# Optimization experiments

Measured on AMD Instinct MI355X. Metric: run time of the kernel, lower is better.

Reference implementation:

```python
import jax, jax.numpy as jnp
import numpy as np
from jax import lax

B, N, C_IN, C_OUT = 8, 8192, 64, 128
NUM_SAMPLES, K = 2048, 32
EPS = 1e-5


def _bn(x, g, b, m, v):
    # inference-mode BatchNorm1d over channel axis 1; x: [G, C, L]
    scale = g / jnp.sqrt(v + EPS)
    return (x - m[None, :, None]) * scale[None, :, None] + b[None, :, None]


def _conv1x1(x, w):
    # kernel_size=1 Conv1d (no bias); x: [G, Cin, L], w: [Cout, Cin]
    return jnp.einsum('gck,oc->gok', x, w)


def _res_block(x, w1, g1, b1, m1, v1, w2, g2, b2, m2, v2):
    # conv-bn-relu -> conv-bn, residual add, relu (residual_factor=1.0)
    y = jax.nn.relu(_bn(_conv1x1(x, w1), g1, b1, m1, v1))
    y = _bn(_conv1x1(y, w2), g2, b2, m2, v2)
    return jax.nn.relu(y + x)


def _fps(xyz, num_samples):
    # farthest point sampling; xyz: [B,N,3] -> indices [B,S]
    b, n, _ = xyz.shape

    def step(carry, _):
        dists, last_idx = carry
        last_pt = jnp.take_along_axis(xyz, last_idx[:, None, None], axis=1)  # [B,1,3]
        d = jnp.sum((xyz - last_pt) ** 2, axis=-1)  # [B,N]
        dists = jnp.minimum(dists, d)
        nxt = jnp.argmax(dists, axis=-1).astype(jnp.int32)
        return (dists, nxt), last_idx

    init = (jnp.full((b, n), 1e10, xyz.dtype), jnp.zeros((b,), jnp.int32))
    _, idxs = lax.scan(step, init, None, length=num_samples)
    return jnp.transpose(idxs)  # [B,S]


def setup_inputs():
    key = jax.random.key(0)
    ks = jax.random.split(key, 40)
    xyz = jax.random.uniform(ks[0], (B, N, 3), jnp.float32)
    feat = jax.random.normal(ks[1], (B, N, C_IN), jnp.float32)

    def conv_w(k, o, c):
        return jax.random.normal(k, (o, c), jnp.float32) * (1.0 / np.sqrt(c).astype(np.float32))

    def bn_params(k, c):
        k1, k2, k3, k4 = jax.random.split(k, 4)
        return (1.0 + 0.1 * jax.random.normal(k1, (c,), jnp.float32),
                0.1 * jax.random.normal(k2, (c,), jnp.float32),
                0.1 * jax.random.normal(k3, (c,), jnp.float32),
                jax.random.uniform(k4, (c,), jnp.float32, 0.5, 1.5))

    inp = {'xyz': xyz, 'feat': feat}
    inp['te_w'] = conv_w(ks[2], C_OUT, 2 * C_IN)
    inp['te_g'], inp['te_b'], inp['te_m'], inp['te_v'] = bn_params(ks[3], C_OUT)
    for name, base in (('pre', 4), ('pos', 14)):
        inp[name + '_w1'] = jnp.stack([conv_w(ks[base + i], C_OUT, C_OUT) for i in range(2)])
        inp[name + '_w2'] = jnp.stack([conv_w(ks[base + 2 + i], C_OUT, C_OUT) for i in range(2)])
        bn1 = [bn_params(ks[base + 4 + i], C_OUT) for i in range(2)]
        bn2 = [bn_params(ks[base + 6 + i], C_OUT) for i in range(2)]
        for j, s in enumerate(('g', 'b', 'm', 'v')):
            inp[f'{name}_{s}1'] = jnp.stack([bn1[i][j] for i in range(2)])
            inp[f'{name}_{s}2'] = jnp.stack([bn2[i][j] for i in range(2)])
    return inp


def reference(xyz, feat, te_w, te_g, te_b, te_m, te_v,
              pre_w1, pre_w2, pre_g1, pre_b1, pre_m1, pre_v1, pre_g2, pre_b2, pre_m2, pre_v2,
              pos_w1, pos_w2, pos_g1, pos_b1, pos_m1, pos_v1, pos_g2, pos_b2, pos_m2, pos_v2):
    bsz = xyz.shape[0]
    # --- LocalGrouper: FPS centers + kNN grouping + concat center feat ---
    fps_idx = _fps(xyz, NUM_SAMPLES)                                    # [B,S]
    new_xyz = jnp.take_along_axis(xyz, fps_idx[..., None], axis=1)      # [B,S,3]
    ctr_feat = jnp.take_along_axis(feat, fps_idx[..., None], axis=1)    # [B,S,C]
    d2 = jnp.sum((new_xyz[:, :, None, :] - xyz[:, None, :, :]) ** 2, axis=-1)  # [B,S,N]
    _, knn_idx = lax.top_k(-d2, K)                                      # [B,S,K]
    grouped = feat[jnp.arange(bsz)[:, None, None], knn_idx]             # [B,S,K,C]
    ctr = jnp.broadcast_to(ctr_feat[:, :, None, :], grouped.shape)
    nf = jnp.concatenate([grouped, ctr], axis=-1)                       # [B,S,K,2C]
    # --- permute/view -> [B*S, 2C, K] ---
    x = nf.transpose(0, 1, 3, 2).reshape(bsz * NUM_SAMPLES, 2 * C_IN, K)
    x = jax.nn.relu(_bn(_conv1x1(x, te_w), te_g, te_b, te_m, te_v))     # [G,OUT,K]
    for i in range(2):
        x = _res_block(x, pre_w1[i], pre_g1[i], pre_b1[i], pre_m1[i], pre_v1[i],
                       pre_w2[i], pre_g2[i], pre_b2[i], pre_m2[i], pre_v2[i])
    x = jnp.max(x, axis=-1)                                             # adaptive_max_pool1d(.,1)
    x = x.reshape(bsz, NUM_SAMPLES, C_OUT).transpose(0, 2, 1)           # [B,OUT,S]
    for i in range(2):
        x = _res_block(x, pos_w1[i], pos_g1[i], pos_b1[i], pos_m1[i], pos_v1[i],
                       pos_w2[i], pos_g2[i], pos_b2[i], pos_m2[i], pos_v2[i])
    return new_xyz, x
```

## Files before the change

kernel.cpp:

```cpp
#include <hip/hip_runtime.h>

typedef unsigned short u16;
typedef unsigned int   u32;
typedef unsigned long long u64;

#define B_    8
#define N_    8192
#define CIN   64
#define COUT  128
#define NS    2048
#define K_    32
#define LDSPAD 136

typedef __attribute__((ext_vector_type(8))) short short8;
typedef __attribute__((ext_vector_type(4))) float f32x4;
typedef __attribute__((ext_vector_type(2))) float f32x2;

#define MFMA16(a,b,c) __builtin_amdgcn_mfma_f32_16x16x32_bf16(a,b,c,0,0,0)

__device__ __forceinline__ u16 f2bf(float f){
  u32 u = __float_as_uint(f);
  return (u16)((u + 0x7FFFu + ((u >> 16) & 1u)) >> 16);
}
__device__ __forceinline__ float bf2f(u16 h){ u32 u = ((u32)h) << 16; return __uint_as_float(u); }
__device__ __forceinline__ u32 pack2bf(float lo, float hi){ return (u32)f2bf(lo) | ((u32)f2bf(hi) << 16); }

__global__ void clear_kernel(int* __restrict__ fps_idx, u32* __restrict__ done,
                             u32* __restrict__ wready){
  int i = blockIdx.x * 256 + threadIdx.x;
  if (i < B_*NS){ fps_idx[i] = -1; done[i] = 0u; }
  if (i == 0) wready[0] = 0u;
}

struct BnPtrs { const float* g[9]; const float* b[9]; const float* m[9]; const float* v[9]; };

struct ShFps {
  u64 key3[3];
  __align__(16) f32x4 cA[2][8];
};
struct ShMid {
  __align__(16) u16 X[8][32*LDSPAD];
  __align__(16) float scr[8][128];
};
struct ShPos {
  __align__(16) u16 X[8][32*LDSPAD];
};
union ShAll { ShFps f; ShMid m; ShPos p; char pad[83968]; };

__device__ __forceinline__ void lds_barrier(){
  __builtin_amdgcn_sched_barrier(0);
  asm volatile("s_waitcnt lgkmcnt(0)\n\ts_barrier" ::: "memory");
  __builtin_amdgcn_sched_barrier(0);
}

#define DPP_UMAX(x, ctrl) { \
  u32 o = (u32)__builtin_amdgcn_update_dpp((int)(x), (int)(x), ctrl, 0xf, 0xf, false); \
  x = (o > x) ? o : x; }

__device__ __forceinline__ u32 wave_umax63(u32 x){
  DPP_UMAX(x, 0x111)
  DPP_UMAX(x, 0x112)
  DPP_UMAX(x, 0x114)
  DPP_UMAX(x, 0x118)
  DPP_UMAX(x, 0x142)
  DPP_UMAX(x, 0x143)
  return (u32)__builtin_amdgcn_readlane((int)x, 63);
}

#define FPS_PAIR(m) { \
  f32x2 dx = PXr##m - lx2; \
  f32x2 dy = PYr##m - ly2; \
  f32x2 dz = PZr##m - lz2; \
  f32x2 t0 = dx*dx; \
  f32x2 t1 = dy*dy; \
  f32x2 t2 = dz*dz; \
  f32x2 dd = (t0 + t1) + t2; \
  f32x2 nd; \
  nd.x = fminf(Dr##m.x, dd.x); \
  nd.y = fminf(Dr##m.y, dd.y); \
  Dr##m = nd; \
  fmA = fmaxf(fmA, nd.x); \
  fmB = fmaxf(fmB, nd.y); }

#define FPS_SELK(m) { \
  if (Dr##m.y == wmf){ kk = 2*m + 1; wx = PXr##m.y; wy = PYr##m.y; wz = PZr##m.y; } \
  if (Dr##m.x == wmf){ kk = 2*m;     wx = PXr##m.x; wy = PYr##m.x; wz = PZr##m.x; } }

__device__ void fps_path(const float* __restrict__ xyz, int* __restrict__ fps_idx,
                         ShFps& S, int b, int t){
  #pragma clang fp contract(off)
  const int lane = t & 63, wv = t >> 6;
  const float* xb = xyz + (size_t)b * N_ * 3;
  const int base = t * 16;
  f32x4 raw0, raw1, raw2, raw3, raw4, raw5, raw6, raw7, raw8, raw9, rawA, rawB;
  {
    const f32x4* xv = (const f32x4*)(xb + (size_t)base * 3);
    raw0 = xv[0]; raw1 = xv[1]; raw2 = xv[2];  raw3 = xv[3];
    raw4 = xv[4]; raw5 = xv[5]; raw6 = xv[6];  raw7 = xv[7];
    raw8 = xv[8]; raw9 = xv[9]; rawA = xv[10]; rawB = xv[11];
  }
  f32x2 PXr0,PXr1,PXr2,PXr3,PXr4,PXr5,PXr6,PXr7;
  f32x2 PYr0,PYr1,PYr2,PYr3,PYr4,PYr5,PYr6,PYr7;
  f32x2 PZr0,PZr1,PZr2,PZr3,PZr4,PZr5,PZr6,PZr7;
  #define GETF(k) (k<4?raw0[(k)&3]:k<8?raw1[(k)&3]:k<12?raw2[(k)&3]:k<16?raw3[(k)&3]: \
                   k<20?raw4[(k)&3]:k<24?raw5[(k)&3]:k<28?raw6[(k)&3]:k<32?raw7[(k)&3]: \
                   k<36?raw8[(k)&3]:k<40?raw9[(k)&3]:k<44?rawA[(k)&3]:rawB[(k)&3])
  #define SETP(m) { \
    PXr##m.x = GETF(6*m+0); PXr##m.y = GETF(6*m+3); \
    PYr##m.x = GETF(6*m+1); PYr##m.y = GETF(6*m+4); \
    PZr##m.x = GETF(6*m+2); PZr##m.y = GETF(6*m+5); }
  SETP(0) SETP(1) SETP(2) SETP(3) SETP(4) SETP(5) SETP(6) SETP(7)
  #undef SETP
  #undef GETF
  if (t == 0){
    S.key3[0] = 0; S.key3[1] = 0; S.key3[2] = 0;
    __hip_atomic_store(fps_idx + b*NS, 0, __ATOMIC_RELAXED, __HIP_MEMORY_SCOPE_AGENT);
  }
  f32x2 Dr0,Dr1,Dr2,Dr3,Dr4,Dr5,Dr6,Dr7;
  Dr0=Dr1=Dr2=Dr3=Dr4=Dr5=Dr6=Dr7=(f32x2){1e10f,1e10f};
  const float sx = xb[0], sy = xb[1], sz = xb[2];
  f32x2 lx2 = {sx,sx}, ly2 = {sy,sy}, lz2 = {sz,sz};
  __syncthreads();
  int my_pi = 0;
  int sl3 = 0, zsl = 1;
  for (int s = 0; s < NS - 1; ++s){
    float fmA = 0.f, fmB = 0.f;
    FPS_PAIR(0) FPS_PAIR(1) FPS_PAIR(2) FPS_PAIR(3)
    FPS_PAIR(4) FPS_PAIR(5) FPS_PAIR(6) FPS_PAIR(7)
    const float fm = fmaxf(fmA, fmB);
    const u32 tbm = __float_as_uint(fm);
    const u32 wmax = wave_umax63(tbm);
    const u64 mask = __ballot(tbm == wmax);
    const int fl = __ffsll((long long)mask) - 1;
    const int sl = s & 1;
    if (lane == fl){
      const float wmf = __uint_as_float(wmax);
      int kk = 0;
      float wx = PXr0.x, wy = PYr0.x, wz = PZr0.x;
      FPS_SELK(7) FPS_SELK(6) FPS_SELK(5) FPS_SELK(4)
      FPS_SELK(3) FPS_SELK(2) FPS_SELK(1) FPS_SELK(0)
      const int pi = base + kk;
      atomicMax((unsigned long long*)&S.key3[sl3],
                ((u64)wmax << 13) | (u64)(8191 - pi));
      f32x4 c; c[0] = wx; c[1] = wy; c[2] = wz; c[3] = 0.f;
      S.cA[sl][wv] = c;
    }
    if (t == 0) S.key3[zsl] = 0;
    lds_barrier();
    const u64 win = S.key3[sl3];
    const int pi_out = 8191 - (int)(win & 0x1FFFull);
    const f32x4 c0 = S.cA[sl][pi_out >> 10];
    lx2.x = c0[0]; lx2.y = c0[0];
    ly2.x = c0[1]; ly2.y = c0[1];
    lz2.x = c0[2]; lz2.y = c0[2];
    if (lane == (s & 15)) my_pi = pi_out;
    if ((s & 15) == 15 && t < 16)
      __hip_atomic_store(fps_idx + b*NS + s - 14 + t, my_pi,
                         __ATOMIC_RELAXED, __HIP_MEMORY_SCOPE_AGENT);
    sl3 = zsl; zsl = (zsl == 2) ? 0 : (zsl + 1);
  }
  if (t < 15)
    __hip_atomic_store(fps_idx + b*NS + (NS - 15) + t, my_pi,
                       __ATOMIC_RELAXED, __HIP_MEMORY_SCOPE_AGENT);
}

__device__ __forceinline__ void st_wt(u32* p, u32 v){
  __hip_atomic_store(p, v, __ATOMIC_RELAXED, __HIP_MEMORY_SCOPE_AGENT);
}

__device__ void prep_path(const float* s_te, const float* s_pre1, const float* s_pre2,
    const float* s_pos1, const float* s_pos2,
    u16* te_w, u16* pre_w1, u16* pre_w2, u16* pos_w1, u16* pos_w2,
    BnPtrs bp, float* bns, u32* wready, int t){
  #define CVT2(src, dst, n) \
    for (int i = t; i < (n)/2; i += 512) \
      st_wt((u32*)(dst) + i, pack2bf((src)[2*i], (src)[2*i+1]));
  CVT2(s_te,   te_w,   16384)
  CVT2(s_pre1, pre_w1, 32768)
  CVT2(s_pre2, pre_w2, 32768)
  CVT2(s_pos1, pos_w1, 32768)
  CVT2(s_pos2, pos_w2, 32768)
  #undef CVT2
  for (int i = t; i < 9*128; i += 512){
    int set = i >> 7, c = i & 127;
    float sc = bp.g[set][c] / sqrtf(bp.v[set][c] + 1e-5f);
    st_wt((u32*)(bns + set*256 + c),       __float_as_uint(sc));
    st_wt((u32*)(bns + set*256 + 128 + c), __float_as_uint(bp.b[set][c] - bp.m[set][c] * sc));
  }
  __syncthreads();
  if (t == 0)
    __hip_atomic_store(wready, 1u, __ATOMIC_RELEASE, __HIP_MEMORY_SCOPE_AGENT);
}

__device__ __forceinline__ void zero_acc(f32x4 acc[8][2]){
  #pragma unroll
  for (int mt = 0; mt < 8; ++mt)
    #pragma unroll
    for (int nt = 0; nt < 2; ++nt){
      acc[mt][nt][0] = 0.f; acc[mt][nt][1] = 0.f; acc[mt][nt][2] = 0.f; acc[mt][nt][3] = 0.f;
    }
}

__device__ __forceinline__ void conv_step(const u16* __restrict__ W, const u16* __restrict__ Xw,
                                          int q, int l15, f32x4 acc[8][2]){
  #pragma unroll
  for (int kk = 0; kk < 4; ++kk){
    short8 b0 = *(const short8*)(Xw + l15*LDSPAD + kk*32 + q*8);
    short8 b1 = *(const short8*)(Xw + (16 + l15)*LDSPAD + kk*32 + q*8);
    #pragma unroll
    for (int mt = 0; mt < 8; ++mt){
      short8 a = *(const short8*)(W + (size_t)(mt*16 + l15)*COUT + kk*32 + q*8);
      acc[mt][0] = MFMA16(a, b0, acc[mt][0]);
      acc[mt][1] = MFMA16(a, b1, acc[mt][1]);
    }
  }
}

__device__ __forceinline__ void res_block(const u16* __restrict__ W1, const u16* __restrict__ W2,
    const float* __restrict__ bn1, const float* __restrict__ bn2,
    u16* __restrict__ Xw, int q, int l15, u32 resid[8][2][2], f32x4 acc[8][2], bool writeback){
  zero_acc(acc);
  conv_step(W1, Xw, q, l15, acc);
  #pragma unroll
  for (int mt = 0; mt < 8; ++mt){
    f32x4 sc = *(const f32x4*)(bn1 + mt*16 + q*4);
    f32x4 bi = *(const f32x4*)(bn1 + 128 + mt*16 + q*4);
    #pragma unroll
    for (int nt = 0; nt < 2; ++nt){
      float y0 = fmaxf(fmaf(acc[mt][nt][0], sc[0], bi[0]), 0.f);
      float y1 = fmaxf(fmaf(acc[mt][nt][1], sc[1], bi[1]), 0.f);
      float y2 = fmaxf(fmaf(acc[mt][nt][2], sc[2], bi[2]), 0.f);
      float y3 = fmaxf(fmaf(acc[mt][nt][3], sc[3], bi[3]), 0.f);
      *(uint2*)(Xw + (nt*16 + l15)*LDSPAD + mt*16 + q*4) = make_uint2(pack2bf(y0,y1), pack2bf(y2,y3));
    }
  }
  __syncthreads();
  zero_acc(acc);
  conv_step(W2, Xw, q, l15, acc);
  #pragma unroll
  for (int mt = 0; mt < 8; ++mt){
    f32x4 sc = *(const f32x4*)(bn2 + mt*16 + q*4);
    f32x4 bi = *(const f32x4*)(bn2 + 128 + mt*16 + q*4);
    #pragma unroll
    for (int nt = 0; nt < 2; ++nt){
      float r0 = bf2f((u16)(resid[mt][nt][0] & 0xFFFFu));
      float r1 = bf2f((u16)(resid[mt][nt][0] >> 16));
      float r2 = bf2f((u16)(resid[mt][nt][1] & 0xFFFFu));
      float r3 = bf2f((u16)(resid[mt][nt][1] >> 16));
      float y0 = fmaxf(fmaf(acc[mt][nt][0], sc[0], bi[0]) + r0, 0.f);
      float y1 = fmaxf(fmaf(acc[mt][nt][1], sc[1], bi[1]) + r1, 0.f);
      float y2 = fmaxf(fmaf(acc[mt][nt][2], sc[2], bi[2]) + r2, 0.f);
      float y3 = fmaxf(fmaf(acc[mt][nt][3], sc[3], bi[3]) + r3, 0.f);
      acc[mt][nt][0] = y0; acc[mt][nt][1] = y1; acc[mt][nt][2] = y2; acc[mt][nt][3] = y3;
      if (writeback){
        u32 p0 = pack2bf(y0,y1), p1 = pack2bf(y2,y3);
        resid[mt][nt][0] = p0; resid[mt][nt][1] = p1;
        *(uint2*)(Xw + (nt*16 + l15)*LDSPAD + mt*16 + q*4) = make_uint2(p0, p1);
      }
    }
  }
  if (writeback) __syncthreads();
}

__device__ void knnmid_path(const float* __restrict__ xyz, const float* __restrict__ feat,
    const u16* __restrict__ te_w, const u16* __restrict__ pre_w1, const u16* __restrict__ pre_w2,
    const float* __restrict__ bns, int* __restrict__ fps_idx,
    u16* __restrict__ x_mid, u32* __restrict__ done, float* __restrict__ out_xyz,
    u16* __restrict__ Xw, float* __restrict__ scrw, int g, int lane){
  #pragma clang fp contract(off)
  const int b = g >> 11;
  const float* xb = xyz + (size_t)b * N_ * 3;

  int raw;
  for (;;){
    raw = __hip_atomic_load(fps_idx + g, __ATOMIC_RELAXED, __HIP_MEMORY_SCOPE_AGENT);
    if (raw >= 0) break;
    __builtin_amdgcn_s_sleep(2);
  }
  const int ci = raw & (N_ - 1);
  const float cx = xb[ci*3], cy = xb[ci*3+1], cz = xb[ci*3+2];
  if (lane < 3) out_xyz[g*3 + lane] = xb[ci*3 + lane];

  float rd = __uint_as_float(0x7F800000u); int ri = 0x7FFFFFFF;
  float r31d = rd; int r31i = ri;
  for (int c = 0; c < N_/64; ++c){
    const int pid = c*64 + lane;
    float dx = xb[pid*3]   - cx;
    float dy = xb[pid*3+1] - cy;
    float dz = xb[pid*3+2] - cz;
    float t0 = dx*dx, t1 = dy*dy, t2 = dz*dz;
    float d2 = (t0 + t1) + t2;
    u64 m = __ballot((d2 < r31d) || (d2 == r31d && pid < r31i));
    while (m){
      int l = __ffsll((long long)m) - 1; m &= m - 1;
      float v = __shfl(d2, l); int vi = c*64 + l;
      if (!((v < r31d) || (v == r31d && vi < r31i))) continue;
      bool lt = (rd < v) || (rd == v && ri < vi);
      int pos = __popcll(__ballot(lt));
      float prd = __shfl_up(rd, 1); int pri = __shfl_up(ri, 1);
      if (lane == pos){ rd = v; ri = vi; }
      else if (lane > pos){ rd = prd; ri = pri; }
      r31d = __shfl(rd, 31); r31i = __shfl(ri, 31);
    }
  }

  const int q = lane >> 4, l15 = lane & 15;
  const float* fb = feat + (size_t)b * N_ * CIN;
  #pragma unroll
  for (int it = 0; it < 4; ++it){
    int lidx = it*64 + lane;
    int kq = lidx & 7;
    int col = it*8 + (lane >> 3);
    int nb = __shfl(ri, col) & (N_ - 1);
    f32x4 a0 = *(const f32x4*)(fb + (size_t)nb*CIN + kq*8);
    f32x4 a1 = *(const f32x4*)(fb + (size_t)nb*CIN + kq*8 + 4);
    *(uint2*)(Xw + col*LDSPAD + kq*8)     = make_uint2(pack2bf(a0[0],a0[1]), pack2bf(a0[2],a0[3]));
    *(uint2*)(Xw + col*LDSPAD + kq*8 + 4) = make_uint2(pack2bf(a1[0],a1[1]), pack2bf(a1[2],a1[3]));
    f32x4 c0 = *(const f32x4*)(fb + (size_t)ci*CIN + kq*8);
    f32x4 c1 = *(const f32x4*)(fb + (size_t)ci*CIN + kq*8 + 4);
    *(uint2*)(Xw + col*LDSPAD + 64 + kq*8)     = make_uint2(pack2bf(c0[0],c0[1]), pack2bf(c0[2],c0[3]));
    *(uint2*)(Xw + col*LDSPAD + 64 + kq*8 + 4) = make_uint2(pack2bf(c1[0],c1[1]), pack2bf(c1[2],c1[3]));
  }
  __syncthreads();

  f32x4 acc[8][2];
  u32 resid[8][2][2];
  zero_acc(acc);
  conv_step(te_w, Xw, q, l15, acc);
  #pragma unroll
  for (int mt = 0; mt < 8; ++mt){
    f32x4 sc = *(const f32x4*)(bns + mt*16 + q*4);
    f32x4 bi = *(const f32x4*)(bns + 128 + mt*16 + q*4);
    #pragma unroll
    for (int nt = 0; nt < 2; ++nt){
      float y0 = fmaxf(fmaf(acc[mt][nt][0], sc[0], bi[0]), 0.f);
      float y1 = fmaxf(fmaf(acc[mt][nt][1], sc[1], bi[1]), 0.f);
      float y2 = fmaxf(fmaf(acc[mt][nt][2], sc[2], bi[2]), 0.f);
      float y3 = fmaxf(fmaf(acc[mt][nt][3], sc[3], bi[3]), 0.f);
      u32 p0 = pack2bf(y0,y1), p1 = pack2bf(y2,y3);
      resid[mt][nt][0] = p0; resid[mt][nt][1] = p1;
      *(uint2*)(Xw + (nt*16 + l15)*LDSPAD + mt*16 + q*4) = make_uint2(p0, p1);
    }
  }
  __syncthreads();

  res_block(pre_w1,             pre_w2,             bns + 256, bns + 512,  Xw, q, l15, resid, acc, true);
  res_block(pre_w1 + COUT*COUT, pre_w2 + COUT*COUT, bns + 768, bns + 1024, Xw, q, l15, resid, acc, false);

  float mx[8][4];
  #pragma unroll
  for (int mt = 0; mt < 8; ++mt)
    #pragma unroll
    for (int r = 0; r < 4; ++r){
      float m0 = fmaxf(acc[mt][0][r], acc[mt][1][r]);
      #pragma unroll
      for (int off = 1; off < 16; off <<= 1) m0 = fmaxf(m0, __shfl_xor(m0, off));
      mx[mt][r] = m0;
    }
  if (l15 == 0){
    #pragma unroll
    for (int mt = 0; mt < 8; ++mt){
      f32x4 vv; vv[0] = mx[mt][0]; vv[1] = mx[mt][1]; vv[2] = mx[mt][2]; vv[3] = mx[mt][3];
      *(f32x4*)(scrw + mt*16 + q*4) = vv;
    }
  }
  __syncthreads();
  float v0 = scrw[lane*2], v1 = scrw[lane*2 + 1];
  *(u32*)(x_mid + (size_t)g*COUT + lane*2) = pack2bf(v0, v1);
  if (lane == 0)
    __hip_atomic_store(done + g, 1u, __ATOMIC_RELEASE, __HIP_MEMORY_SCOPE_AGENT);
}

__device__ void pos_path(const u16* __restrict__ x_mid,
    const u16* __restrict__ pos_w1, const u16* __restrict__ pos_w2,
    const float* __restrict__ bns, float* __restrict__ out_x,
    u32* __restrict__ done, u16* __restrict__ Xw, int g, int lane){
  const int q = lane >> 4, l15 = lane & 15;
  const int gc0 = g * 32;
  const int b = gc0 >> 11, s0 = gc0 & 2047;
  for (;;){
    u32 d = (lane < 32)
      ? __hip_atomic_load(done + gc0 + lane, __ATOMIC_RELAXED, __HIP_MEMORY_SCOPE_AGENT)
      : 1u;
    if (__all(d != 0)) break;
    __builtin_amdgcn_s_sleep(16);
  }
  __builtin_amdgcn_fence(__ATOMIC_ACQUIRE, "agent");
  #pragma unroll
  for (int it = 0; it < 8; ++it){
    int lidx = it*64 + lane;
    int col = lidx >> 4, kq = lidx & 15;
    uint4 v = *(const uint4*)(x_mid + (size_t)(gc0 + col)*COUT + kq*8);
    *(uint4*)(Xw + col*LDSPAD + kq*8) = v;
  }
  __syncthreads();
  u32 resid[8][2][2];
  #pragma unroll
  for (int mt = 0; mt < 8; ++mt)
    #pragma unroll
    for (int nt = 0; nt < 2; ++nt){
      uint2 rr = *(const uint2*)(Xw + (nt*16 + l15)*LDSPAD + mt*16 + q*4);
      resid[mt][nt][0] = rr.x; resid[mt][nt][1] = rr.y;
    }
  f32x4 acc[8][2];
  res_block(pos_w1,             pos_w2,             bns + 1280, bns + 1536, Xw, q, l15, resid, acc, true);
  res_block(pos_w1 + COUT*COUT, pos_w2 + COUT*COUT, bns + 1792, bns + 2048, Xw, q, l15, resid, acc, false);
  #pragma unroll
  for (int mt = 0; mt < 8; ++mt)
    #pragma unroll
    for (int nt = 0; nt < 2; ++nt)
      #pragma unroll
      for (int r = 0; r < 4; ++r){
        int row = mt*16 + q*4 + r;
        int colx = s0 + nt*16 + l15;
        out_x[(size_t)(b*COUT + row)*NS + colx] = acc[mt][nt][r];
      }
}

#define GRID_FPS    B_
#define GRID_PREP   1
#define GRID_KM     (B_*NS/8)
#define GRID_POS    (B_*NS/K_/8)

__global__ __launch_bounds__(512) void mega_kernel(
    const float* __restrict__ xyz, const float* __restrict__ feat,
    const float* __restrict__ s_te, const float* __restrict__ s_pre1,
    const float* __restrict__ s_pre2, const float* __restrict__ s_pos1,
    const float* __restrict__ s_pos2, BnPtrs bp,
    u16* __restrict__ te_w, u16* __restrict__ pre_w1, u16* __restrict__ pre_w2,
    u16* __restrict__ pos_w1, u16* __restrict__ pos_w2,
    float* __restrict__ bns, int* __restrict__ fps_idx,
    u16* __restrict__ x_mid, u32* __restrict__ done, u32* __restrict__ wready,
    float* __restrict__ out_xyz, float* __restrict__ out_x){
  __shared__ ShAll sh;
  const int bid = blockIdx.x;
  const int t = threadIdx.x;
  const int wid = t >> 6, lane = t & 63;
  if (bid < GRID_FPS){
    fps_path(xyz, fps_idx, sh.f, bid, t);
  } else if (bid < GRID_FPS + GRID_PREP){
    prep_path(s_te, s_pre1, s_pre2, s_pos1, s_pos2,
              te_w, pre_w1, pre_w2, pos_w1, pos_w2, bp, bns, wready, t);
  } else if (bid < GRID_FPS + GRID_PREP + GRID_KM){
    const int i = bid - GRID_FPS - GRID_PREP;
    const int g0 = (i & 7) * NS + (i >> 3) * 8;
    if (t == 0){
      while (__hip_atomic_load(wready, __ATOMIC_RELAXED, __HIP_MEMORY_SCOPE_AGENT) == 0u ||
             __hip_atomic_load(fps_idx + g0 + 7, __ATOMIC_RELAXED,
                               __HIP_MEMORY_SCOPE_AGENT) < 0)
        __builtin_amdgcn_s_sleep(16);
    }
    __syncthreads();
    knnmid_path(xyz, feat, te_w, pre_w1, pre_w2, bns, fps_idx, x_mid, done, out_xyz,
                sh.m.X[wid], sh.m.scr[wid], g0 + wid, lane);
  } else {
    const int idx = (bid - GRID_FPS - GRID_PREP - GRID_KM)*8 + wid;
    const int g = (idx & 7) * (NS/K_) + (idx >> 3);
    pos_path(x_mid, pos_w1, pos_w2, bns, out_x, done, sh.p.X[wid], g, lane);
  }
}

extern "C" void kernel_launch(void* const* d_in, const int* in_sizes, int n_in,
                              void* d_out, int out_size, void* d_ws, size_t ws_size,
                              hipStream_t stream){
  (void)in_sizes; (void)n_in; (void)out_size; (void)ws_size;
  const float* xyz    = (const float*)d_in[0];
  const float* feat   = (const float*)d_in[1];

  char* ws = (char*)d_ws;
  float* bns     = (float*)ws;
  u32*   wready  = (u32*)(ws + 12288);
  u16*   wbf     = (u16*)(ws + 16384);
  int*   fps_idx = (int*)(ws + 16384 + 294912);
  u32*   done    = (u32*)(ws + 16384 + 294912 + 65536);
  u16*   x_mid   = (u16*)(ws + 16384 + 294912 + 65536 + 65536);
  float* out_xyz = (float*)d_out;
  float* out_x   = (float*)d_out + B_*NS*3;

  u16* te_w   = wbf;
  u16* pre_w1 = wbf + 16384;
  u16* pre_w2 = wbf + 49152;
  u16* pos_w1 = wbf + 81920;
  u16* pos_w2 = wbf + 114688;

  BnPtrs bp;
  const int gi[9] = {3, 9, 10, 9, 10, 19, 20, 19, 20};
  const int bbi[9]= {4, 11,12, 11,12, 21, 22, 21, 22};
  const int mi[9] = {5, 13,14, 13,14, 23, 24, 23, 24};
  const int vi[9] = {6, 15,16, 15,16, 25, 26, 25, 26};
  const int of[9] = {0, 0, 0, 128,128, 0, 0, 128,128};
  for (int k = 0; k < 9; ++k){
    bp.g[k] = (const float*)d_in[gi[k]]  + of[k];
    bp.b[k] = (const float*)d_in[bbi[k]] + of[k];
    bp.m[k] = (const float*)d_in[mi[k]]  + of[k];
    bp.v[k] = (const float*)d_in[vi[k]]  + of[k];
  }

  clear_kernel<<<64, 256, 0, stream>>>(fps_idx, done, wready);
  mega_kernel<<<GRID_FPS + GRID_PREP + GRID_KM + GRID_POS, 512, 0, stream>>>(
      xyz, feat,
      (const float*)d_in[2], (const float*)d_in[7], (const float*)d_in[8],
      (const float*)d_in[17], (const float*)d_in[18], bp,
      te_w, pre_w1, pre_w2, pos_w1, pos_w2,
      bns, fps_idx, x_mid, done, wready, out_xyz, out_x);
}
```

Baseline: 2.827 ms.

## Halve active FPS threads, giving each thread 32 points in registers

```diff
diff --git a/kernel.cpp b/kernel.cpp
--- a/kernel.cpp
+++ b/kernel.cpp
@@ -89,35 +89,40 @@
 __device__ void fps_path(const float* __restrict__ xyz, int* __restrict__ fps_idx,
                          ShFps& S, int b, int t){
   #pragma clang fp contract(off)
+  if (t >= 256){
+    __syncthreads();
+    for (int s = 0; s < NS - 1; ++s) lds_barrier();
+    return;
+  }
   const int lane = t & 63, wv = t >> 6;
   const float* xb = xyz + (size_t)b * N_ * 3;
-  const int base = t * 16;
-  f32x4 raw0, raw1, raw2, raw3, raw4, raw5, raw6, raw7, raw8, raw9, rawA, rawB;
+  const int base = t * 32;
+  f32x2 PXr0,PXr1,PXr2,PXr3,PXr4,PXr5,PXr6,PXr7;
+  f32x2 PXr8,PXr9,PXr10,PXr11,PXr12,PXr13,PXr14,PXr15;
+  f32x2 PYr0,PYr1,PYr2,PYr3,PYr4,PYr5,PYr6,PYr7;
+  f32x2 PYr8,PYr9,PYr10,PYr11,PYr12,PYr13,PYr14,PYr15;
+  f32x2 PZr0,PZr1,PZr2,PZr3,PZr4,PZr5,PZr6,PZr7;
+  f32x2 PZr8,PZr9,PZr10,PZr11,PZr12,PZr13,PZr14,PZr15;
   {
     const f32x4* xv = (const f32x4*)(xb + (size_t)base * 3);
-    raw0 = xv[0]; raw1 = xv[1]; raw2 = xv[2];  raw3 = xv[3];
-    raw4 = xv[4]; raw5 = xv[5]; raw6 = xv[6];  raw7 = xv[7];
-    raw8 = xv[8]; raw9 = xv[9]; rawA = xv[10]; rawB = xv[11];
-  }
-  f32x2 PXr0,PXr1,PXr2,PXr3,PXr4,PXr5,PXr6,PXr7;
-  f32x2 PYr0,PYr1,PYr2,PYr3,PYr4,PYr5,PYr6,PYr7;
-  f32x2 PZr0,PZr1,PZr2,PZr3,PZr4,PZr5,PZr6,PZr7;
-  #define GETF(k) (k<4?raw0[(k)&3]:k<8?raw1[(k)&3]:k<12?raw2[(k)&3]:k<16?raw3[(k)&3]: \
-                   k<20?raw4[(k)&3]:k<24?raw5[(k)&3]:k<28?raw6[(k)&3]:k<32?raw7[(k)&3]: \
-                   k<36?raw8[(k)&3]:k<40?raw9[(k)&3]:k<44?rawA[(k)&3]:rawB[(k)&3])
-  #define SETP(m) { \
-    PXr##m.x = GETF(6*m+0); PXr##m.y = GETF(6*m+3); \
-    PYr##m.x = GETF(6*m+1); PYr##m.y = GETF(6*m+4); \
-    PZr##m.x = GETF(6*m+2); PZr##m.y = GETF(6*m+5); }
-  SETP(0) SETP(1) SETP(2) SETP(3) SETP(4) SETP(5) SETP(6) SETP(7)
-  #undef SETP
-  #undef GETF
+    #define LOADC(c, a, bq) { \
+      f32x4 r0 = xv[3*c], r1 = xv[3*c+1], r2 = xv[3*c+2]; \
+      PXr##a.x  = r0[0]; PYr##a.x  = r0[1]; PZr##a.x  = r0[2]; \
+      PXr##a.y  = r0[3]; PYr##a.y  = r1[0]; PZr##a.y  = r1[1]; \
+      PXr##bq.x = r1[2]; PYr##bq.x = r1[3]; PZr##bq.x = r2[0]; \
+      PXr##bq.y = r2[1]; PYr##bq.y = r2[2]; PZr##bq.y = r2[3]; }
+    LOADC(0,0,1)  LOADC(1,2,3)  LOADC(2,4,5)   LOADC(3,6,7)
+    LOADC(4,8,9)  LOADC(5,10,11) LOADC(6,12,13) LOADC(7,14,15)
+    #undef LOADC
+  }
   if (t == 0){
     S.key3[0] = 0; S.key3[1] = 0; S.key3[2] = 0;
     __hip_atomic_store(fps_idx + b*NS, 0, __ATOMIC_RELAXED, __HIP_MEMORY_SCOPE_AGENT);
   }
   f32x2 Dr0,Dr1,Dr2,Dr3,Dr4,Dr5,Dr6,Dr7;
+  f32x2 Dr8,Dr9,Dr10,Dr11,Dr12,Dr13,Dr14,Dr15;
   Dr0=Dr1=Dr2=Dr3=Dr4=Dr5=Dr6=Dr7=(f32x2){1e10f,1e10f};
+  Dr8=Dr9=Dr10=Dr11=Dr12=Dr13=Dr14=Dr15=(f32x2){1e10f,1e10f};
   const float sx = xb[0], sy = xb[1], sz = xb[2];
   f32x2 lx2 = {sx,sx}, ly2 = {sy,sy}, lz2 = {sz,sz};
   __syncthreads();
@@ -125,8 +130,10 @@
   int sl3 = 0, zsl = 1;
   for (int s = 0; s < NS - 1; ++s){
     float fmA = 0.f, fmB = 0.f;
-    FPS_PAIR(0) FPS_PAIR(1) FPS_PAIR(2) FPS_PAIR(3)
-    FPS_PAIR(4) FPS_PAIR(5) FPS_PAIR(6) FPS_PAIR(7)
+    FPS_PAIR(0)  FPS_PAIR(1)  FPS_PAIR(2)  FPS_PAIR(3)
+    FPS_PAIR(4)  FPS_PAIR(5)  FPS_PAIR(6)  FPS_PAIR(7)
+    FPS_PAIR(8)  FPS_PAIR(9)  FPS_PAIR(10) FPS_PAIR(11)
+    FPS_PAIR(12) FPS_PAIR(13) FPS_PAIR(14) FPS_PAIR(15)
     const float fm = fmaxf(fmA, fmB);
     const u32 tbm = __float_as_uint(fm);
     const u32 wmax = wave_umax63(tbm);
@@ -137,8 +144,10 @@
       const float wmf = __uint_as_float(wmax);
       int kk = 0;
       float wx = PXr0.x, wy = PYr0.x, wz = PZr0.x;
-      FPS_SELK(7) FPS_SELK(6) FPS_SELK(5) FPS_SELK(4)
-      FPS_SELK(3) FPS_SELK(2) FPS_SELK(1) FPS_SELK(0)
+      FPS_SELK(15) FPS_SELK(14) FPS_SELK(13) FPS_SELK(12)
+      FPS_SELK(11) FPS_SELK(10) FPS_SELK(9)  FPS_SELK(8)
+      FPS_SELK(7)  FPS_SELK(6)  FPS_SELK(5)  FPS_SELK(4)
+      FPS_SELK(3)  FPS_SELK(2)  FPS_SELK(1)  FPS_SELK(0)
       const int pi = base + kk;
       atomicMax((unsigned long long*)&S.key3[sl3],
                 ((u64)wmax << 13) | (u64)(8191 - pi));
@@ -149,7 +158,7 @@
     lds_barrier();
     const u64 win = S.key3[sl3];
     const int pi_out = 8191 - (int)(win & 0x1FFFull);
-    const f32x4 c0 = S.cA[sl][pi_out >> 10];
+    const f32x4 c0 = S.cA[sl][pi_out >> 11];
     lx2.x = c0[0]; lx2.y = c0[0];
     ly2.x = c0[1]; ly2.y = c0[1];
     lz2.x = c0[2]; lz2.y = c0[2];
```

Result: slower. 3.043 ms (+7.7%).

## Replace FPS LDS atomicMax with per-wave keys and make consumer blocks persistent

Applied to the files above, without the earlier changes.

```diff
diff --git a/kernel.cpp b/kernel.cpp
--- a/kernel.cpp
+++ b/kernel.cpp
@@ -35,7 +35,7 @@
 struct BnPtrs { const float* g[9]; const float* b[9]; const float* m[9]; const float* v[9]; };
 
 struct ShFps {
-  u64 key3[3];
+  __align__(16) u64  keyA[2][8];
   __align__(16) f32x4 cA[2][8];
 };
 struct ShMid {
@@ -86,6 +86,12 @@
   if (Dr##m.y == wmf){ kk = 2*m + 1; wx = PXr##m.y; wy = PYr##m.y; wz = PZr##m.y; } \
   if (Dr##m.x == wmf){ kk = 2*m;     wx = PXr##m.x; wy = PYr##m.x; wz = PZr##m.x; } }
 
+__device__ __forceinline__ void selmax(u64& ka, f32x4& ca, u64 kb, f32x4 cb){
+  bool c = kb > ka;
+  ka = c ? kb : ka;
+  ca = c ? cb : ca;
+}
+
 __device__ void fps_path(const float* __restrict__ xyz, int* __restrict__ fps_idx,
                          ShFps& S, int b, int t){
   #pragma clang fp contract(off)
@@ -112,17 +118,13 @@
   SETP(0) SETP(1) SETP(2) SETP(3) SETP(4) SETP(5) SETP(6) SETP(7)
   #undef SETP
   #undef GETF
-  if (t == 0){
-    S.key3[0] = 0; S.key3[1] = 0; S.key3[2] = 0;
+  if (t == 0)
     __hip_atomic_store(fps_idx + b*NS, 0, __ATOMIC_RELAXED, __HIP_MEMORY_SCOPE_AGENT);
-  }
   f32x2 Dr0,Dr1,Dr2,Dr3,Dr4,Dr5,Dr6,Dr7;
   Dr0=Dr1=Dr2=Dr3=Dr4=Dr5=Dr6=Dr7=(f32x2){1e10f,1e10f};
   const float sx = xb[0], sy = xb[1], sz = xb[2];
   f32x2 lx2 = {sx,sx}, ly2 = {sy,sy}, lz2 = {sz,sz};
-  __syncthreads();
   int my_pi = 0;
-  int sl3 = 0, zsl = 1;
   for (int s = 0; s < NS - 1; ++s){
     float fmA = 0.f, fmB = 0.f;
     FPS_PAIR(0) FPS_PAIR(1) FPS_PAIR(2) FPS_PAIR(3)
@@ -140,24 +142,26 @@
       FPS_SELK(7) FPS_SELK(6) FPS_SELK(5) FPS_SELK(4)
       FPS_SELK(3) FPS_SELK(2) FPS_SELK(1) FPS_SELK(0)
       const int pi = base + kk;
-      atomicMax((unsigned long long*)&S.key3[sl3],
-                ((u64)wmax << 13) | (u64)(8191 - pi));
+      S.keyA[sl][wv] = ((u64)wmax << 13) | (u64)(8191 - pi);
       f32x4 c; c[0] = wx; c[1] = wy; c[2] = wz; c[3] = 0.f;
       S.cA[sl][wv] = c;
     }
-    if (t == 0) S.key3[zsl] = 0;
     lds_barrier();
-    const u64 win = S.key3[sl3];
-    const int pi_out = 8191 - (int)(win & 0x1FFFull);
-    const f32x4 c0 = S.cA[sl][pi_out >> 10];
+    u64 k0 = S.keyA[sl][0], k1 = S.keyA[sl][1], k2 = S.keyA[sl][2], k3 = S.keyA[sl][3];
+    u64 k4 = S.keyA[sl][4], k5 = S.keyA[sl][5], k6 = S.keyA[sl][6], k7 = S.keyA[sl][7];
+    f32x4 c0 = S.cA[sl][0], c1 = S.cA[sl][1], c2 = S.cA[sl][2], c3 = S.cA[sl][3];
+    f32x4 c4 = S.cA[sl][4], c5 = S.cA[sl][5], c6 = S.cA[sl][6], c7 = S.cA[sl][7];
+    selmax(k0,c0,k1,c1); selmax(k2,c2,k3,c3); selmax(k4,c4,k5,c5); selmax(k6,c6,k7,c7);
+    selmax(k0,c0,k2,c2); selmax(k4,c4,k6,c6);
+    selmax(k0,c0,k4,c4);
     lx2.x = c0[0]; lx2.y = c0[0];
     ly2.x = c0[1]; ly2.y = c0[1];
     lz2.x = c0[2]; lz2.y = c0[2];
+    const int pi_out = 8191 - (int)(k0 & 0x1FFFull);
     if (lane == (s & 15)) my_pi = pi_out;
     if ((s & 15) == 15 && t < 16)
       __hip_atomic_store(fps_idx + b*NS + s - 14 + t, my_pi,
                          __ATOMIC_RELAXED, __HIP_MEMORY_SCOPE_AGENT);
-    sl3 = zsl; zsl = (zsl == 2) ? 0 : (zsl + 1);
   }
   if (t < 15)
     __hip_atomic_store(fps_idx + b*NS + (NS - 15) + t, my_pi,
@@ -419,8 +423,10 @@
 
 #define GRID_FPS    B_
 #define GRID_PREP   1
-#define GRID_KM     (B_*NS/8)
-#define GRID_POS    (B_*NS/K_/8)
+#define GRID_KM_BLK 96
+#define KM_UNITS    (B_*NS/8)
+#define GRID_POS_BLK 16
+#define POS_UNITS   (B_*NS/K_/8)
 
 __global__ __launch_bounds__(512) void mega_kernel(
     const float* __restrict__ xyz, const float* __restrict__ feat,
@@ -441,22 +447,29 @@
   } else if (bid < GRID_FPS + GRID_PREP){
     prep_path(s_te, s_pre1, s_pre2, s_pos1, s_pos2,
               te_w, pre_w1, pre_w2, pos_w1, pos_w2, bp, bns, wready, t);
-  } else if (bid < GRID_FPS + GRID_PREP + GRID_KM){
-    const int i = bid - GRID_FPS - GRID_PREP;
-    const int g0 = (i & 7) * NS + (i >> 3) * 8;
-    if (t == 0){
-      while (__hip_atomic_load(wready, __ATOMIC_RELAXED, __HIP_MEMORY_SCOPE_AGENT) == 0u ||
-             __hip_atomic_load(fps_idx + g0 + 7, __ATOMIC_RELAXED,
-                               __HIP_MEMORY_SCOPE_AGENT) < 0)
-        __builtin_amdgcn_s_sleep(16);
-    }
-    __syncthreads();
-    knnmid_path(xyz, feat, te_w, pre_w1, pre_w2, bns, fps_idx, x_mid, done, out_xyz,
-                sh.m.X[wid], sh.m.scr[wid], g0 + wid, lane);
+  } else if (bid < GRID_FPS + GRID_PREP + GRID_KM_BLK){
+    const int ib = bid - GRID_FPS - GRID_PREP;
+    for (int j = ib; j < KM_UNITS; j += GRID_KM_BLK){
+      const int g0 = (j & 7) * NS + (j >> 3) * 8;
+      if (t == 0){
+        while (__hip_atomic_load(wready, __ATOMIC_RELAXED, __HIP_MEMORY_SCOPE_AGENT) == 0u ||
+               __hip_atomic_load(fps_idx + g0 + 7, __ATOMIC_RELAXED,
+                                 __HIP_MEMORY_SCOPE_AGENT) < 0)
+          __builtin_amdgcn_s_sleep(16);
+      }
+      __syncthreads();
+      knnmid_path(xyz, feat, te_w, pre_w1, pre_w2, bns, fps_idx, x_mid, done, out_xyz,
+                  sh.m.X[wid], sh.m.scr[wid], g0 + wid, lane);
+      __syncthreads();
+    }
   } else {
-    const int idx = (bid - GRID_FPS - GRID_PREP - GRID_KM)*8 + wid;
-    const int g = (idx & 7) * (NS/K_) + (idx >> 3);
-    pos_path(x_mid, pos_w1, pos_w2, bns, out_x, done, sh.p.X[wid], g, lane);
+    const int ib = bid - GRID_FPS - GRID_PREP - GRID_KM_BLK;
+    for (int j = ib; j < POS_UNITS; j += GRID_POS_BLK){
+      const int idx = j*8 + wid;
+      const int g = (idx & 7) * (NS/K_) + (idx >> 3);
+      pos_path(x_mid, pos_w1, pos_w2, bns, out_x, done, sh.p.X[wid], g, lane);
+      __syncthreads();
+    }
   }
 }
 
@@ -497,7 +510,7 @@
   }
 
   clear_kernel<<<64, 256, 0, stream>>>(fps_idx, done, wready);
-  mega_kernel<<<GRID_FPS + GRID_PREP + GRID_KM + GRID_POS, 512, 0, stream>>>(
+  mega_kernel<<<GRID_FPS + GRID_PREP + GRID_KM_BLK + GRID_POS_BLK, 512, 0, stream>>>(
       xyz, feat,
       (const float*)d_in[2], (const float*)d_in[7], (const float*)d_in[8],
       (const float*)d_in[17], (const float*)d_in[18], bp,
```

Result: slower. 3.494 ms (+23.6%).
